# Kernel optimization log

Hardware: AMD Instinct MI355X
Metric: run time of the kernel (lower is better)

## Reference

```python
import jax, jax.numpy as jnp
import numpy as np

N = 100000      # nodes
E = 1600000     # edges (avg degree 16)
F_IN = 128
HID = 64
OUT = 40
NB = 10000      # batch_nodes
BN_EPS = 1e-5


def setup_inputs() -> dict:
    key = jax.random.key(0)
    ks = jax.random.split(key, 16)
    inp = {}
    inp["features"] = jax.random.normal(ks[0], (N, F_IN), dtype=jnp.float32)
    inp["edge_index"] = jax.random.randint(ks[1], (2, E), 0, N, dtype=jnp.int32)
    inp["batch_nodes"] = jax.random.randint(ks[2], (NB,), 0, N, dtype=jnp.int32)
    # conv1 params (Glorot-ish scale)
    inp["W1"] = jax.random.normal(ks[3], (F_IN, HID), dtype=jnp.float32) * (1.0 / np.sqrt(F_IN))
    inp["b1"] = jnp.zeros((HID,), jnp.float32)
    inp["k2_1"] = jnp.float32(0.5)   # learnable k^2, init 0.5
    # conv2 params
    inp["W2"] = jax.random.normal(ks[4], (HID, OUT), dtype=jnp.float32) * (1.0 / np.sqrt(HID))
    inp["b2"] = jnp.zeros((OUT,), jnp.float32)
    inp["k2_2"] = jnp.float32(0.5)
    # BatchNorm1d(hid) inference params
    inp["g1"] = jax.random.uniform(ks[5], (HID,), jnp.float32, 0.5, 1.5)
    inp["be1"] = jax.random.normal(ks[6], (HID,), jnp.float32) * 0.1
    inp["m1"] = jax.random.normal(ks[7], (HID,), jnp.float32) * 0.1
    inp["v1"] = jax.random.uniform(ks[8], (HID,), jnp.float32, 0.5, 1.5)
    # BatchNorm1d(out) inference params
    inp["g2"] = jax.random.uniform(ks[9], (OUT,), jnp.float32, 0.5, 1.5)
    inp["be2"] = jax.random.normal(ks[10], (OUT,), jnp.float32) * 0.1
    inp["m2"] = jax.random.normal(ks[11], (OUT,), jnp.float32) * 0.1
    inp["v2"] = jax.random.uniform(ks[12], (OUT,), jnp.float32, 0.5, 1.5)
    return inp


def _gcn_propagate(h, src, dst, n):
    # add self loops
    loop = jnp.arange(n, dtype=src.dtype)
    s = jnp.concatenate([src, loop])
    d = jnp.concatenate([dst, loop])
    # symmetric GCN normalization D^-1/2 A_hat D^-1/2
    deg = jnp.zeros((n,), h.dtype).at[d].add(1.0)
    dinv = jax.lax.rsqrt(deg)  # deg >= 1 thanks to self loops
    coef = dinv[s] * dinv[d]   # [E+N]
    msg = coef[:, None] * h[s]                      # gather  [E+N, C]
    agg = jnp.zeros_like(h).at[d].add(msg)          # scatter [N, C]
    return agg


def _helm_conv(x, W, b, k2, src, dst, n):
    h = x @ W                                   # [N, C_out]
    agg = _gcn_propagate(h, src, dst, n)        # A_hat h
    out = agg + k2 * h + b                      # (A_hat + k^2 I) h + b
    # Helmholtz residual: (A_hat - I + k^2 I) h ~ (-L + k^2) h
    resid = agg - h + k2 * h
    helm_loss = jnp.mean(resid * resid)
    return out, helm_loss


def _bn(x, g, be, m, v):
    return (x - m) * jax.lax.rsqrt(v + BN_EPS) * g + be


def reference(features, edge_index, batch_nodes, W1, b1, k2_1, W2, b2, k2_2,
              g1, be1, m1, v1, g2, be2, m2, v2):
    n = features.shape[0]
    src, dst = edge_index[0], edge_index[1]
    x, helm_loss1 = _helm_conv(features, W1, b1, k2_1, src, dst, n)
    x = jnp.tanh(_bn(x, g1, be1, m1, v1))
    # dropout is identity in eval mode
    x, _ = _helm_conv(x, W2, b2, k2_2, src, dst, n)
    x = jnp.tanh(_bn(x, g2, be2, m2, v2))
    logp = jax.nn.log_softmax(x[batch_nodes], axis=1)
    return (logp, helm_loss1)
```

## Files before the change

kernel.cpp:

```cpp
#include <hip/hip_runtime.h>
#include <math.h>


#define BN_EPS 1e-5f
#define NB_BKT 512
#define RCAP 4608
#define PSTRIDE 8448

typedef __attribute__((ext_vector_type(8))) short bf16x8;
typedef __attribute__((ext_vector_type(4))) float f32x4;

__device__ inline unsigned short f2b(float f) {
    unsigned u = __float_as_uint(f);
    unsigned r = (u + 0x7fffu + ((u >> 16) & 1u)) >> 16;
    return (unsigned short)r;
}
__device__ inline float b2f_lo(unsigned u) { return __uint_as_float(u << 16); }
__device__ inline float b2f_hi(unsigned u) { return __uint_as_float(u & 0xffff0000u); }
__device__ inline unsigned pk2(float a, float b) {
    return (unsigned)f2b(a) | ((unsigned)f2b(b) << 16);
}
__device__ inline float tanh_fast(float x) {
    float e = __expf(2.0f * x);
    return 1.0f - 2.0f * __builtin_amdgcn_rcpf(e + 1.0f);
}
__device__ inline float qcoef(unsigned q) {
    return __uint_as_float((q >> 1) & 0xFFFF0000u);
}

__global__ __launch_bounds__(256) void k_part(const int* __restrict__ src,
                                              const int* __restrict__ dst, int e,
                                              unsigned* __restrict__ bcnt,
                                              unsigned* __restrict__ part, int nblk) {
    __shared__ unsigned h[NB_BKT];
    __shared__ unsigned gbase[NB_BKT];
    __shared__ unsigned cur[NB_BKT];
    int chunk = ((e + nblk - 1) / nblk + 3) & ~3;
    int c0 = blockIdx.x * chunk;
    int c1 = min(c0 + chunk, e);
    if (c0 >= e) return;
    for (int i = threadIdx.x; i < NB_BKT; i += 256) h[i] = 0;
    __syncthreads();
    for (int i = c0 + threadIdx.x * 4; i < c1; i += 1024) {
        if (i + 3 < c1) {
            int4 d = *(const int4*)&dst[i];
            atomicAdd(&h[(unsigned)d.x >> 8], 1u);
            atomicAdd(&h[(unsigned)d.y >> 8], 1u);
            atomicAdd(&h[(unsigned)d.z >> 8], 1u);
            atomicAdd(&h[(unsigned)d.w >> 8], 1u);
        } else {
            for (int j = i; j < c1; ++j) atomicAdd(&h[(unsigned)dst[j] >> 8], 1u);
        }
    }
    __syncthreads();
    for (int i = threadIdx.x; i < NB_BKT; i += 256) {
        unsigned c = h[i];
        gbase[i] = c ? (i * RCAP + atomicAdd(&bcnt[i], c)) : 0u;
        cur[i] = 0;
    }
    __syncthreads();
    for (int i = c0 + threadIdx.x * 4; i < c1; i += 1024) {
        if (i + 3 < c1) {
            int4 s = *(const int4*)&src[i];
            int4 d = *(const int4*)&dst[i];
            unsigned b0 = (unsigned)d.x >> 8, b1 = (unsigned)d.y >> 8;
            unsigned b2 = (unsigned)d.z >> 8, b3 = (unsigned)d.w >> 8;
            unsigned p0 = gbase[b0] + atomicAdd(&cur[b0], 1u);
            unsigned p1 = gbase[b1] + atomicAdd(&cur[b1], 1u);
            unsigned p2 = gbase[b2] + atomicAdd(&cur[b2], 1u);
            unsigned p3 = gbase[b3] + atomicAdd(&cur[b3], 1u);
            if (p0 < (b0 + 1) * RCAP) part[p0] = (((unsigned)d.x & 255u) << 24) | (unsigned)s.x;
            if (p1 < (b1 + 1) * RCAP) part[p1] = (((unsigned)d.y & 255u) << 24) | (unsigned)s.y;
            if (p2 < (b2 + 1) * RCAP) part[p2] = (((unsigned)d.z & 255u) << 24) | (unsigned)s.z;
            if (p3 < (b3 + 1) * RCAP) part[p3] = (((unsigned)d.w & 255u) << 24) | (unsigned)s.w;
        } else {
            for (int j = i; j < c1; ++j) {
                unsigned b = (unsigned)dst[j] >> 8;
                unsigned p = gbase[b] + atomicAdd(&cur[b], 1u);
                if (p < (b + 1) * RCAP)
                    part[p] = (((unsigned)dst[j] & 255u) << 24) | (unsigned)src[j];
            }
        }
    }
}

__global__ __launch_bounds__(256) void k_deg(const unsigned* __restrict__ part,
                                             const unsigned* __restrict__ bcnt,
                                             unsigned long long* __restrict__ rowinfo,
                                             float* __restrict__ dinv, int n,
                                             const float* __restrict__ b1,
                                             const float* __restrict__ g1,
                                             const float* __restrict__ be1,
                                             const float* __restrict__ m1,
                                             const float* __restrict__ v1,
                                             const float* __restrict__ b2p,
                                             const float* __restrict__ g2,
                                             const float* __restrict__ be2,
                                             const float* __restrict__ m2,
                                             const float* __restrict__ v2,
                                             float* __restrict__ A1,
                                             float* __restrict__ S1,
                                             float* __restrict__ A2,
                                             float* __restrict__ S2) {
    __shared__ unsigned hist[256];
    __shared__ unsigned sc[256];
    int b = blockIdx.x;
    int cnt = (int)min(bcnt[b], (unsigned)RCAP);
    unsigned base = b * RCAP;
    int dst0 = b << 8;
    int nloc = min(256, n - dst0);
    int t = threadIdx.x;
    hist[t] = 0;
    __syncthreads();
    for (int i = t; i < cnt; i += 256) atomicAdd(&hist[part[base + i] >> 24], 1u);
    __syncthreads();
    unsigned c = hist[t];
    unsigned pcnt = (t < nloc) ? ((c + 15u) & ~15u) : 0u;
    sc[t] = pcnt;
    __syncthreads();
    for (int off = 1; off < 256; off <<= 1) {
        unsigned a = (t >= off) ? sc[t - off] : 0u;
        __syncthreads();
        sc[t] += a;
        __syncthreads();
    }
    if (t < nloc) {
        unsigned beg = (unsigned)b * PSTRIDE + (sc[t] - pcnt);
        rowinfo[dst0 + t] = (unsigned long long)beg | ((unsigned long long)pcnt << 32);
        dinv[dst0 + t] = rsqrtf((float)(c + 1u));
    }
    if (b == 0) {
        if (t < 64) {
            float a = g1[t] * rsqrtf(v1[t] + BN_EPS);
            A1[t] = a;
            S1[t] = (b1[t] - m1[t]) * a + be1[t];
        } else if (t < 104) {
            int cc = t - 64;
            float a = g2[cc] * rsqrtf(v2[cc] + BN_EPS);
            A2[cc] = a;
            S2[cc] = (b2p[cc] - m2[cc]) * a + be2[cc];
        }
    }
}

__global__ __launch_bounds__(256) void k_scatter(const unsigned* __restrict__ part,
                                                 const unsigned* __restrict__ bcnt,
                                                 const unsigned long long* __restrict__ rowinfo,
                                                 const float* __restrict__ dinv,
                                                 unsigned* __restrict__ qs, int n) {
    __shared__ unsigned cur[256];
    __shared__ unsigned pend[256];
    int b = blockIdx.x;
    int cnt = (int)min(bcnt[b], (unsigned)RCAP);
    unsigned base = b * RCAP;
    int dst0 = b << 8;
    int nloc = min(256, n - dst0);
    int t = threadIdx.x;
    if (t < nloc) {
        unsigned long long ri = rowinfo[dst0 + t];
        cur[t] = (unsigned)ri;
        pend[t] = (unsigned)ri + (unsigned)(ri >> 32);
    } else {
        cur[t] = 0;
        pend[t] = 0;
    }
    __syncthreads();
    for (int i = t; i < cnt; i += 256) {
        unsigned p = part[base + i];
        unsigned loc = p >> 24;
        unsigned s = p & 0xFFFFFFu;
        unsigned du = __float_as_uint(dinv[s]);
        unsigned q = (((du + 0x8000u) & 0xFFFF0000u) << 1) | s;
        unsigned pos = atomicAdd(&cur[loc], 1u);
        qs[pos] = q;
    }
    __syncthreads();
    if (t < nloc) {
        for (unsigned pos = cur[t]; pos < pend[t]; ++pos) qs[pos] = 0u;
    }
}

__global__ __launch_bounds__(256) void k_gemm1(const float* __restrict__ X,
                                               const float* __restrict__ W,
                                               unsigned* __restrict__ H, int n) {
    __shared__ short wb[4][4][64][8];
    __shared__ float cbuf[4][16][65];
    int t = threadIdx.x;
    for (int s = t; s < 1024; s += 256) {
        int l = s & 63, nt = (s >> 6) & 3, kt = s >> 8;
        int kbase = kt * 32 + ((l >> 4) << 3);
        int nn = nt * 16 + (l & 15);
        bf16x8 v;
#pragma unroll
        for (int j = 0; j < 8; ++j) v[j] = (short)f2b(W[(kbase + j) * 64 + nn]);
        *(bf16x8*)&wb[kt][nt][l][0] = v;
    }
    __syncthreads();
    int lane = t & 63, wave = t >> 6;
    int quad = lane >> 4, m = lane & 15;
    int r0 = blockIdx.x * 64 + wave * 16;
    f32x4 acc[4];
#pragma unroll
    for (int i = 0; i < 4; ++i) acc[i] = (f32x4){0.f, 0.f, 0.f, 0.f};
    int rr = min(r0 + m, n - 1);
    const float* xrow = X + (size_t)rr * 128;
#pragma unroll
    for (int kt = 0; kt < 4; ++kt) {
        int kb = kt * 32 + quad * 8;
        float4 x0 = *(const float4*)&xrow[kb];
        float4 x1 = *(const float4*)&xrow[kb + 4];
        bf16x8 af;
        af[0] = (short)f2b(x0.x); af[1] = (short)f2b(x0.y);
        af[2] = (short)f2b(x0.z); af[3] = (short)f2b(x0.w);
        af[4] = (short)f2b(x1.x); af[5] = (short)f2b(x1.y);
        af[6] = (short)f2b(x1.z); af[7] = (short)f2b(x1.w);
#pragma unroll
        for (int nt = 0; nt < 4; ++nt) {
            bf16x8 bf = *(bf16x8*)&wb[kt][nt][lane][0];
            acc[nt] = __builtin_amdgcn_mfma_f32_16x16x32_bf16(af, bf, acc[nt], 0, 0, 0);
        }
    }
#pragma unroll
    for (int nt = 0; nt < 4; ++nt)
#pragma unroll
        for (int r = 0; r < 4; ++r)
            cbuf[wave][quad * 4 + r][nt * 16 + m] = acc[nt][r];
    __syncthreads();
#pragma unroll
    for (int i = 0; i < 8; ++i) {
        int f = i * 64 + lane;
        int row = f >> 5, cp = f & 31;
        int grow = r0 + row;
        if (grow < n)
            H[(size_t)grow * 32 + cp] =
                pk2(cbuf[wave][row][2 * cp], cbuf[wave][row][2 * cp + 1]);
    }
}

__global__ __launch_bounds__(256) void k_gemm2(const unsigned short* __restrict__ X,
                                               const float* __restrict__ W,
                                               unsigned* __restrict__ H, int n) {
    __shared__ short wb[2][3][64][8];
    __shared__ float cbuf[4][16][49];
    int t = threadIdx.x;
    for (int s = t; s < 384; s += 256) {
        int l = s & 63, nt = (s >> 6) % 3, kt = s / 192;
        int kbase = kt * 32 + ((l >> 4) << 3);
        int c = nt * 16 + (l & 15);
        bf16x8 v;
#pragma unroll
        for (int j = 0; j < 8; ++j)
            v[j] = (c < 40) ? (short)f2b(W[(kbase + j) * 40 + c]) : (short)0;
        *(bf16x8*)&wb[kt][nt][l][0] = v;
    }
    __syncthreads();
    int lane = t & 63, wave = t >> 6;
    int quad = lane >> 4, m = lane & 15;
    int r0 = blockIdx.x * 64 + wave * 16;
    f32x4 acc[3];
#pragma unroll
    for (int i = 0; i < 3; ++i) acc[i] = (f32x4){0.f, 0.f, 0.f, 0.f};
    int rr = min(r0 + m, n - 1);
    const unsigned short* xrow = X + (size_t)rr * 64;
#pragma unroll
    for (int kt = 0; kt < 2; ++kt) {
        bf16x8 af = *(const bf16x8*)&xrow[kt * 32 + quad * 8];
#pragma unroll
        for (int nt = 0; nt < 3; ++nt) {
            bf16x8 bf = *(bf16x8*)&wb[kt][nt][lane][0];
            acc[nt] = __builtin_amdgcn_mfma_f32_16x16x32_bf16(af, bf, acc[nt], 0, 0, 0);
        }
    }
#pragma unroll
    for (int nt = 0; nt < 3; ++nt)
#pragma unroll
        for (int r = 0; r < 4; ++r)
            cbuf[wave][quad * 4 + r][nt * 16 + m] = acc[nt][r];
    __syncthreads();
#pragma unroll
    for (int i = 0; i < 5; ++i) {
        int f = i * 64 + lane;
        int row = f / 20, cp = f % 20;
        int grow = r0 + row;
        if (grow < n)
            H[(size_t)grow * 20 + cp] =
                pk2(cbuf[wave][row][2 * cp], cbuf[wave][row][2 * cp + 1]);
    }
}

__global__ __launch_bounds__(256) void k_conv1(const unsigned long long* __restrict__ rowinfo,
                                               const unsigned* __restrict__ qs,
                                               const float* __restrict__ dinv,
                                               const unsigned* __restrict__ h1,
                                               unsigned* __restrict__ x,
                                               const float* __restrict__ A1,
                                               const float* __restrict__ S1,
                                               const float* __restrict__ k2p,
                                               float* __restrict__ partial, int n) {
    int lane = threadIdx.x & 63, wave = threadIdx.x >> 6;
    int half = lane >> 5, c2 = lane & 31;
    int node = __builtin_amdgcn_readfirstlane(blockIdx.x * 4 + wave);
    float r2 = 0.0f;
    if (node < n) {
        unsigned long long ri = rowinfo[node];
        unsigned beg = (unsigned)ri, pdeg = (unsigned)(ri >> 32);
        float dd = dinv[node];
        unsigned hp = h1[(unsigned)node * 32u + (unsigned)c2];
        float hx = b2f_lo(hp), hy = b2f_hi(hp);
        float ax = half ? 0.f : dd * hx;
        float ay = half ? 0.f : dd * hy;
        for (unsigned eb = 0; eb < pdeg; eb += 16) {
            unsigned bi = beg + eb + (unsigned)half * 8u;
            uint4 q0 = *(const uint4*)&qs[bi];
            uint4 q1 = *(const uint4*)&qs[bi + 4];
            unsigned p0 = h1[((q0.x & 0x1FFFFu) << 5) + (unsigned)c2];
            unsigned p1 = h1[((q0.y & 0x1FFFFu) << 5) + (unsigned)c2];
            unsigned p2 = h1[((q0.z & 0x1FFFFu) << 5) + (unsigned)c2];
            unsigned p3 = h1[((q0.w & 0x1FFFFu) << 5) + (unsigned)c2];
            unsigned p4 = h1[((q1.x & 0x1FFFFu) << 5) + (unsigned)c2];
            unsigned p5 = h1[((q1.y & 0x1FFFFu) << 5) + (unsigned)c2];
            unsigned p6 = h1[((q1.z & 0x1FFFFu) << 5) + (unsigned)c2];
            unsigned p7 = h1[((q1.w & 0x1FFFFu) << 5) + (unsigned)c2];
            float c0 = qcoef(q0.x), c1 = qcoef(q0.y), c2f = qcoef(q0.z), c3 = qcoef(q0.w);
            float c4 = qcoef(q1.x), c5 = qcoef(q1.y), c6 = qcoef(q1.z), c7 = qcoef(q1.w);
            ax += c0 * b2f_lo(p0); ay += c0 * b2f_hi(p0);
            ax += c1 * b2f_lo(p1); ay += c1 * b2f_hi(p1);
            ax += c2f * b2f_lo(p2); ay += c2f * b2f_hi(p2);
            ax += c3 * b2f_lo(p3); ay += c3 * b2f_hi(p3);
            ax += c4 * b2f_lo(p4); ay += c4 * b2f_hi(p4);
            ax += c5 * b2f_lo(p5); ay += c5 * b2f_hi(p5);
            ax += c6 * b2f_lo(p6); ay += c6 * b2f_hi(p6);
            ax += c7 * b2f_lo(p7); ay += c7 * b2f_hi(p7);
        }
        ax += __shfl_xor(ax, 32, 64);
        ay += __shfl_xor(ay, 32, 64);
        if (half == 0) {
            float a_x = dd * ax, a_y = dd * ay;
            float k2 = k2p[0];
            float rx = a_x + (k2 - 1.0f) * hx;
            float ry = a_y + (k2 - 1.0f) * hy;
            r2 = rx * rx + ry * ry;
            float2 Ap = *(const float2*)&A1[2 * c2];
            float2 Sp = *(const float2*)&S1[2 * c2];
            float xnx = tanh_fast((a_x + k2 * hx) * Ap.x + Sp.x);
            float xny = tanh_fast((a_y + k2 * hy) * Ap.y + Sp.y);
            x[(unsigned)node * 32u + (unsigned)c2] = pk2(xnx, xny);
        }
    }
    for (int off = 32; off; off >>= 1) r2 += __shfl_xor(r2, off, 64);
    __shared__ float red[4];
    if (lane == 0) red[wave] = r2;
    __syncthreads();
    if (threadIdx.x == 0) partial[blockIdx.x] = red[0] + red[1] + red[2] + red[3];
}

__global__ __launch_bounds__(256) void k_conv2(const int* __restrict__ bn,
                                               const unsigned long long* __restrict__ rowinfo,
                                               const unsigned* __restrict__ qs,
                                               const float* __restrict__ dinv,
                                               const unsigned* __restrict__ h2,
                                               const float* __restrict__ A2,
                                               const float* __restrict__ S2,
                                               const float* __restrict__ k2p,
                                               const float* __restrict__ partial,
                                               int nparts, float inv_cnt,
                                               float* __restrict__ out, int nb) {
    int lane = threadIdx.x & 63, wave = threadIdx.x >> 6;
    if (blockIdx.x == gridDim.x - 1) {
        float s = 0.f;
        for (int i = threadIdx.x; i < nparts; i += 256) s += partial[i];
        for (int off = 32; off; off >>= 1) s += __shfl_xor(s, off, 64);
        __shared__ float red[4];
        if (lane == 0) red[wave] = s;
        __syncthreads();
        if (threadIdx.x == 0)
            out[(size_t)nb * 40] = (red[0] + red[1] + red[2] + red[3]) * inv_cnt;
        return;
    }
    int wid = blockIdx.x * 4 + wave;
    if (wid >= nb) return;
    int half = lane >> 5, c2 = lane & 31;
    unsigned p = (unsigned)min(c2, 19);
    int node = bn[wid];
    unsigned long long ri = rowinfo[node];
    unsigned beg = (unsigned)ri, pdeg = (unsigned)(ri >> 32);
    float dd = dinv[node];
    unsigned hp = h2[(unsigned)node * 20u + p];
    float hx = b2f_lo(hp), hy = b2f_hi(hp);
    float ax = half ? 0.f : dd * hx;
    float ay = half ? 0.f : dd * hy;
    for (unsigned eb = 0; eb < pdeg; eb += 16) {
        unsigned bi = beg + eb + (unsigned)half * 8u;
        uint4 q0 = *(const uint4*)&qs[bi];
        uint4 q1 = *(const uint4*)&qs[bi + 4];
        unsigned p0 = h2[(q0.x & 0x1FFFFu) * 20u + p];
        unsigned p1 = h2[(q0.y & 0x1FFFFu) * 20u + p];
        unsigned p2 = h2[(q0.z & 0x1FFFFu) * 20u + p];
        unsigned p3 = h2[(q0.w & 0x1FFFFu) * 20u + p];
        unsigned p4 = h2[(q1.x & 0x1FFFFu) * 20u + p];
        unsigned p5 = h2[(q1.y & 0x1FFFFu) * 20u + p];
        unsigned p6 = h2[(q1.z & 0x1FFFFu) * 20u + p];
        unsigned p7 = h2[(q1.w & 0x1FFFFu) * 20u + p];
        float c0 = qcoef(q0.x), c1 = qcoef(q0.y), c2f = qcoef(q0.z), c3 = qcoef(q0.w);
        float c4 = qcoef(q1.x), c5 = qcoef(q1.y), c6 = qcoef(q1.z), c7 = qcoef(q1.w);
        ax += c0 * b2f_lo(p0); ay += c0 * b2f_hi(p0);
        ax += c1 * b2f_lo(p1); ay += c1 * b2f_hi(p1);
        ax += c2f * b2f_lo(p2); ay += c2f * b2f_hi(p2);
        ax += c3 * b2f_lo(p3); ay += c3 * b2f_hi(p3);
        ax += c4 * b2f_lo(p4); ay += c4 * b2f_hi(p4);
        ax += c5 * b2f_lo(p5); ay += c5 * b2f_hi(p5);
        ax += c6 * b2f_lo(p6); ay += c6 * b2f_hi(p6);
        ax += c7 * b2f_lo(p7); ay += c7 * b2f_hi(p7);
    }
    ax += __shfl_xor(ax, 32, 64);
    ay += __shfl_xor(ay, 32, 64);
    float k2 = k2p[0];
    float2 Ap = *(const float2*)&A2[2 * p];
    float2 Sp = *(const float2*)&S2[2 * p];
    float tx = tanh_fast((dd * ax + k2 * hx) * Ap.x + Sp.x);
    float ty = tanh_fast((dd * ay + k2 * hy) * Ap.y + Sp.y);
    bool act = (half == 0) && (c2 < 20);
    float mx = act ? fmaxf(tx, ty) : -INFINITY;
    for (int off = 32; off; off >>= 1) mx = fmaxf(mx, __shfl_xor(mx, off, 64));
    float es = act ? (__expf(tx - mx) + __expf(ty - mx)) : 0.f;
    for (int off = 32; off; off >>= 1) es += __shfl_xor(es, off, 64);
    if (act) {
        float ls = mx + __logf(es);
        float2 o = make_float2(tx - ls, ty - ls);
        *(float2*)&out[(size_t)wid * 40 + 2 * p] = o;
    }
}

extern "C" void kernel_launch(void* const* d_in, const int* in_sizes, int n_in,
                              void* d_out, int out_size, void* d_ws, size_t ws_size,
                              hipStream_t stream) {
    const float* features = (const float*)d_in[0];
    const int* edge_index = (const int*)d_in[1];
    const int* batch_nodes = (const int*)d_in[2];
    const float* W1 = (const float*)d_in[3];
    const float* b1 = (const float*)d_in[4];
    const float* k2_1 = (const float*)d_in[5];
    const float* W2 = (const float*)d_in[6];
    const float* b2 = (const float*)d_in[7];
    const float* k2_2 = (const float*)d_in[8];
    const float* g1 = (const float*)d_in[9];
    const float* be1 = (const float*)d_in[10];
    const float* m1 = (const float*)d_in[11];
    const float* v1 = (const float*)d_in[12];
    const float* g2 = (const float*)d_in[13];
    const float* be2 = (const float*)d_in[14];
    const float* m2 = (const float*)d_in[15];
    const float* v2 = (const float*)d_in[16];

    const int N = in_sizes[0] / 128;
    const int E = in_sizes[1] / 2;
    const int NB = in_sizes[2];
    const int* src = edge_index;
    const int* dst = edge_index + E;
    const int NPART = (N + 3) / 4;
    const int NBKT = (N + 255) >> 8;
    const int PBLK = 512;

    unsigned* ws = (unsigned*)d_ws;
    auto align64 = [](size_t o) { return (o + 63) & ~(size_t)63; };
    size_t o = 0;
    unsigned long long* rowinfo = (unsigned long long*)(ws + o); o = align64(o + 2 * (size_t)N);
    float* dinv = (float*)(ws + o);       o = align64(o + N);
    float* A1 = (float*)(ws + o);         o = align64(o + 64);
    float* S1 = (float*)(ws + o);         o = align64(o + 64);
    float* A2 = (float*)(ws + o);         o = align64(o + 64);
    float* S2 = (float*)(ws + o);         o = align64(o + 64);
    unsigned* bcnt = ws + o;              o = align64(o + NB_BKT);
    float* partial = (float*)(ws + o);    o = align64(o + NPART);
    unsigned* qs = ws + o;                o = align64(o + (size_t)NB_BKT * PSTRIDE);
    unsigned* h1 = ws + o;                o = align64(o + (size_t)N * 32);
    unsigned* x = ws + o;                 o = align64(o + (size_t)N * 32);
    unsigned* h2 = ws + o;                o = align64(o + (size_t)N * 20);
    unsigned* part = h1;

    hipMemsetAsync(bcnt, 0, NB_BKT * sizeof(unsigned), stream);
    k_part<<<PBLK, 256, 0, stream>>>(src, dst, E, bcnt, part, PBLK);
    k_deg<<<NBKT, 256, 0, stream>>>(part, bcnt, rowinfo, dinv, N, b1, g1, be1, m1,
                                    v1, b2, g2, be2, m2, v2, A1, S1, A2, S2);
    k_scatter<<<NBKT, 256, 0, stream>>>(part, bcnt, rowinfo, dinv, qs, N);

    k_gemm1<<<(N + 63) / 64, 256, 0, stream>>>(features, W1, h1, N);
    k_conv1<<<NPART, 256, 0, stream>>>(rowinfo, qs, dinv, h1, x, A1, S1, k2_1,
                                       partial, N);
    k_gemm2<<<(N + 63) / 64, 256, 0, stream>>>((const unsigned short*)x, W2, h2, N);
    k_conv2<<<(NB + 3) / 4 + 1, 256, 0, stream>>>(batch_nodes, rowinfo, qs, dinv, h2,
                                                  A2, S2, k2_2, partial, NPART,
                                                  1.0f / ((float)N * 64.0f),
                                                  (float*)d_out, NB);
}
```

Measured before the change: 259.6 us.

## Fuse edge scatter with gemm1 and shrink per-node padding in aggregation

Merges the edge scatter kernel and the first GEMM into one launch whose leading blocks do the scatter and whose remaining blocks do the GEMM. This requires giving the partition buffer its own workspace region instead of aliasing h1. Per-node edge padding drops from multiples of 16 to multiples of 4, and both conv kernels are restructured: conv1 assigns a 16-lane group per node, and conv2 assigns a half-wave per batch node. The goal is to cut wasted padded-edge work and a kernel boundary. The cost is narrower per-node loops with less memory-level parallelism per thread, and fewer partition blocks.

```diff
diff --git a/kernel.cpp b/kernel.cpp
--- a/kernel.cpp
+++ b/kernel.cpp
@@ -5,7 +5,7 @@
 #define BN_EPS 1e-5f
 #define NB_BKT 512
 #define RCAP 4608
-#define PSTRIDE 8448
+#define PSTRIDE 5376
 
 typedef __attribute__((ext_vector_type(8))) short bf16x8;
 typedef __attribute__((ext_vector_type(4))) float f32x4;
@@ -115,7 +115,7 @@
     for (int i = t; i < cnt; i += 256) atomicAdd(&hist[part[base + i] >> 24], 1u);
     __syncthreads();
     unsigned c = hist[t];
-    unsigned pcnt = (t < nloc) ? ((c + 15u) & ~15u) : 0u;
+    unsigned pcnt = (t < nloc) ? ((c + 3u) & ~3u) : 0u;
     sc[t] = pcnt;
     __syncthreads();
     for (int off = 1; off < 256; off <<= 1) {
@@ -143,49 +143,48 @@
     }
 }
 
-__global__ __launch_bounds__(256) void k_scatter(const unsigned* __restrict__ part,
-                                                 const unsigned* __restrict__ bcnt,
-                                                 const unsigned long long* __restrict__ rowinfo,
-                                                 const float* __restrict__ dinv,
-                                                 unsigned* __restrict__ qs, int n) {
-    __shared__ unsigned cur[256];
-    __shared__ unsigned pend[256];
-    int b = blockIdx.x;
-    int cnt = (int)min(bcnt[b], (unsigned)RCAP);
-    unsigned base = b * RCAP;
-    int dst0 = b << 8;
-    int nloc = min(256, n - dst0);
+__global__ __launch_bounds__(256) void k_scatter_gemm1(
+        const unsigned* __restrict__ part, const unsigned* __restrict__ bcnt,
+        const unsigned long long* __restrict__ rowinfo,
+        const float* __restrict__ dinv, unsigned* __restrict__ qs,
+        const float* __restrict__ X, const float* __restrict__ W,
+        unsigned* __restrict__ H, int n, int nbkt) {
+    __shared__ union {
+        struct { unsigned cur[256]; unsigned pend[256]; } s;
+        struct { short wb[4][4][64][8]; float cbuf[4][16][65]; } g;
+    } u;
     int t = threadIdx.x;
-    if (t < nloc) {
-        unsigned long long ri = rowinfo[dst0 + t];
-        cur[t] = (unsigned)ri;
-        pend[t] = (unsigned)ri + (unsigned)(ri >> 32);
-    } else {
-        cur[t] = 0;
-        pend[t] = 0;
-    }
-    __syncthreads();
-    for (int i = t; i < cnt; i += 256) {
-        unsigned p = part[base + i];
-        unsigned loc = p >> 24;
-        unsigned s = p & 0xFFFFFFu;
-        unsigned du = __float_as_uint(dinv[s]);
-        unsigned q = (((du + 0x8000u) & 0xFFFF0000u) << 1) | s;
-        unsigned pos = atomicAdd(&cur[loc], 1u);
-        qs[pos] = q;
-    }
-    __syncthreads();
-    if (t < nloc) {
-        for (unsigned pos = cur[t]; pos < pend[t]; ++pos) qs[pos] = 0u;
-    }
-}
-
-__global__ __launch_bounds__(256) void k_gemm1(const float* __restrict__ X,
-                                               const float* __restrict__ W,
-                                               unsigned* __restrict__ H, int n) {
-    __shared__ short wb[4][4][64][8];
-    __shared__ float cbuf[4][16][65];
-    int t = threadIdx.x;
+    if (blockIdx.x < (unsigned)nbkt) {
+        int b = blockIdx.x;
+        int cnt = (int)min(bcnt[b], (unsigned)RCAP);
+        unsigned base = b * RCAP;
+        int dst0 = b << 8;
+        int nloc = min(256, n - dst0);
+        if (t < nloc) {
+            unsigned long long ri = rowinfo[dst0 + t];
+            u.s.cur[t] = (unsigned)ri;
+            u.s.pend[t] = (unsigned)ri + (unsigned)(ri >> 32);
+        } else {
+            u.s.cur[t] = 0;
+            u.s.pend[t] = 0;
+        }
+        __syncthreads();
+        for (int i = t; i < cnt; i += 256) {
+            unsigned p = part[base + i];
+            unsigned loc = p >> 24;
+            unsigned s = p & 0xFFFFFFu;
+            unsigned du = __float_as_uint(dinv[s]);
+            unsigned q = (((du + 0x8000u) & 0xFFFF0000u) << 1) | s;
+            unsigned pos = atomicAdd(&u.s.cur[loc], 1u);
+            qs[pos] = q;
+        }
+        __syncthreads();
+        if (t < nloc) {
+            for (unsigned pos = u.s.cur[t]; pos < u.s.pend[t]; ++pos) qs[pos] = 0u;
+        }
+        return;
+    }
+    int bid = blockIdx.x - nbkt;
     for (int s = t; s < 1024; s += 256) {
         int l = s & 63, nt = (s >> 6) & 3, kt = s >> 8;
         int kbase = kt * 32 + ((l >> 4) << 3);
@@ -193,12 +192,12 @@
         bf16x8 v;
 #pragma unroll
         for (int j = 0; j < 8; ++j) v[j] = (short)f2b(W[(kbase + j) * 64 + nn]);
-        *(bf16x8*)&wb[kt][nt][l][0] = v;
+        *(bf16x8*)&u.g.wb[kt][nt][l][0] = v;
     }
     __syncthreads();
     int lane = t & 63, wave = t >> 6;
     int quad = lane >> 4, m = lane & 15;
-    int r0 = blockIdx.x * 64 + wave * 16;
+    int r0 = bid * 64 + wave * 16;
     f32x4 acc[4];
 #pragma unroll
     for (int i = 0; i < 4; ++i) acc[i] = (f32x4){0.f, 0.f, 0.f, 0.f};
@@ -216,7 +215,7 @@
         af[6] = (short)f2b(x1.z); af[7] = (short)f2b(x1.w);
 #pragma unroll
         for (int nt = 0; nt < 4; ++nt) {
-            bf16x8 bf = *(bf16x8*)&wb[kt][nt][lane][0];
+            bf16x8 bf = *(bf16x8*)&u.g.wb[kt][nt][lane][0];
             acc[nt] = __builtin_amdgcn_mfma_f32_16x16x32_bf16(af, bf, acc[nt], 0, 0, 0);
         }
     }
@@ -224,7 +223,7 @@
     for (int nt = 0; nt < 4; ++nt)
 #pragma unroll
         for (int r = 0; r < 4; ++r)
-            cbuf[wave][quad * 4 + r][nt * 16 + m] = acc[nt][r];
+            u.g.cbuf[wave][quad * 4 + r][nt * 16 + m] = acc[nt][r];
     __syncthreads();
 #pragma unroll
     for (int i = 0; i < 8; ++i) {
@@ -233,7 +232,7 @@
         int grow = r0 + row;
         if (grow < n)
             H[(size_t)grow * 32 + cp] =
-                pk2(cbuf[wave][row][2 * cp], cbuf[wave][row][2 * cp + 1]);
+                pk2(u.g.cbuf[wave][row][2 * cp], u.g.cbuf[wave][row][2 * cp + 1]);
     }
 }
 
@@ -297,61 +296,58 @@
                                                const float* __restrict__ S1,
                                                const float* __restrict__ k2p,
                                                float* __restrict__ partial, int n) {
-    int lane = threadIdx.x & 63, wave = threadIdx.x >> 6;
-    int half = lane >> 5, c2 = lane & 31;
-    int node = __builtin_amdgcn_readfirstlane(blockIdx.x * 4 + wave);
+    int t = threadIdx.x;
+    int lane = t & 63, wave = t >> 6;
+    int quarter = lane >> 4, cl = lane & 15;
+    int node = blockIdx.x * 16 + wave * 4 + quarter;
     float r2 = 0.0f;
     if (node < n) {
         unsigned long long ri = rowinfo[node];
         unsigned beg = (unsigned)ri, pdeg = (unsigned)(ri >> 32);
         float dd = dinv[node];
-        unsigned hp = h1[(unsigned)node * 32u + (unsigned)c2];
-        float hx = b2f_lo(hp), hy = b2f_hi(hp);
-        float ax = half ? 0.f : dd * hx;
-        float ay = half ? 0.f : dd * hy;
-        for (unsigned eb = 0; eb < pdeg; eb += 16) {
-            unsigned bi = beg + eb + (unsigned)half * 8u;
-            uint4 q0 = *(const uint4*)&qs[bi];
-            uint4 q1 = *(const uint4*)&qs[bi + 4];
-            unsigned p0 = h1[((q0.x & 0x1FFFFu) << 5) + (unsigned)c2];
-            unsigned p1 = h1[((q0.y & 0x1FFFFu) << 5) + (unsigned)c2];
-            unsigned p2 = h1[((q0.z & 0x1FFFFu) << 5) + (unsigned)c2];
-            unsigned p3 = h1[((q0.w & 0x1FFFFu) << 5) + (unsigned)c2];
-            unsigned p4 = h1[((q1.x & 0x1FFFFu) << 5) + (unsigned)c2];
-            unsigned p5 = h1[((q1.y & 0x1FFFFu) << 5) + (unsigned)c2];
-            unsigned p6 = h1[((q1.z & 0x1FFFFu) << 5) + (unsigned)c2];
-            unsigned p7 = h1[((q1.w & 0x1FFFFu) << 5) + (unsigned)c2];
-            float c0 = qcoef(q0.x), c1 = qcoef(q0.y), c2f = qcoef(q0.z), c3 = qcoef(q0.w);
-            float c4 = qcoef(q1.x), c5 = qcoef(q1.y), c6 = qcoef(q1.z), c7 = qcoef(q1.w);
-            ax += c0 * b2f_lo(p0); ay += c0 * b2f_hi(p0);
-            ax += c1 * b2f_lo(p1); ay += c1 * b2f_hi(p1);
-            ax += c2f * b2f_lo(p2); ay += c2f * b2f_hi(p2);
-            ax += c3 * b2f_lo(p3); ay += c3 * b2f_hi(p3);
-            ax += c4 * b2f_lo(p4); ay += c4 * b2f_hi(p4);
-            ax += c5 * b2f_lo(p5); ay += c5 * b2f_hi(p5);
-            ax += c6 * b2f_lo(p6); ay += c6 * b2f_hi(p6);
-            ax += c7 * b2f_lo(p7); ay += c7 * b2f_hi(p7);
-        }
-        ax += __shfl_xor(ax, 32, 64);
-        ay += __shfl_xor(ay, 32, 64);
-        if (half == 0) {
-            float a_x = dd * ax, a_y = dd * ay;
-            float k2 = k2p[0];
-            float rx = a_x + (k2 - 1.0f) * hx;
-            float ry = a_y + (k2 - 1.0f) * hy;
-            r2 = rx * rx + ry * ry;
-            float2 Ap = *(const float2*)&A1[2 * c2];
-            float2 Sp = *(const float2*)&S1[2 * c2];
-            float xnx = tanh_fast((a_x + k2 * hx) * Ap.x + Sp.x);
-            float xny = tanh_fast((a_y + k2 * hy) * Ap.y + Sp.y);
-            x[(unsigned)node * 32u + (unsigned)c2] = pk2(xnx, xny);
-        }
+        uint2 hp = *(const uint2*)&h1[(unsigned)node * 32u + 2u * cl];
+        float h0 = b2f_lo(hp.x), h1v = b2f_hi(hp.x);
+        float h2v = b2f_lo(hp.y), h3 = b2f_hi(hp.y);
+        float a0 = dd * h0, a1 = dd * h1v, a2 = dd * h2v, a3 = dd * h3;
+        for (unsigned eb = 0; eb < pdeg; eb += 4) {
+            uint4 q = *(const uint4*)&qs[beg + eb];
+            unsigned i0 = (q.x & 0x1FFFFu) << 5, i1 = (q.y & 0x1FFFFu) << 5;
+            unsigned i2 = (q.z & 0x1FFFFu) << 5, i3 = (q.w & 0x1FFFFu) << 5;
+            uint2 p0 = *(const uint2*)&h1[i0 + 2u * cl];
+            uint2 p1 = *(const uint2*)&h1[i1 + 2u * cl];
+            uint2 p2 = *(const uint2*)&h1[i2 + 2u * cl];
+            uint2 p3 = *(const uint2*)&h1[i3 + 2u * cl];
+            float c0 = qcoef(q.x), c1 = qcoef(q.y), c2 = qcoef(q.z), c3 = qcoef(q.w);
+            a0 += c0 * b2f_lo(p0.x); a1 += c0 * b2f_hi(p0.x);
+            a2 += c0 * b2f_lo(p0.y); a3 += c0 * b2f_hi(p0.y);
+            a0 += c1 * b2f_lo(p1.x); a1 += c1 * b2f_hi(p1.x);
+            a2 += c1 * b2f_lo(p1.y); a3 += c1 * b2f_hi(p1.y);
+            a0 += c2 * b2f_lo(p2.x); a1 += c2 * b2f_hi(p2.x);
+            a2 += c2 * b2f_lo(p2.y); a3 += c2 * b2f_hi(p2.y);
+            a0 += c3 * b2f_lo(p3.x); a1 += c3 * b2f_hi(p3.x);
+            a2 += c3 * b2f_lo(p3.y); a3 += c3 * b2f_hi(p3.y);
+        }
+        float k2 = k2p[0];
+        float g0 = dd * a0, g1v = dd * a1, g2v = dd * a2, g3 = dd * a3;
+        float r0 = g0 + (k2 - 1.0f) * h0, r1 = g1v + (k2 - 1.0f) * h1v;
+        float r2c = g2v + (k2 - 1.0f) * h2v, r3 = g3 + (k2 - 1.0f) * h3;
+        r2 = r0 * r0 + r1 * r1 + r2c * r2c + r3 * r3;
+        float4 Ap = *(const float4*)&A1[4 * cl];
+        float4 Sp = *(const float4*)&S1[4 * cl];
+        float x0 = tanh_fast((g0 + k2 * h0) * Ap.x + Sp.x);
+        float x1 = tanh_fast((g1v + k2 * h1v) * Ap.y + Sp.y);
+        float x2 = tanh_fast((g2v + k2 * h2v) * Ap.z + Sp.z);
+        float x3 = tanh_fast((g3 + k2 * h3) * Ap.w + Sp.w);
+        uint2 o;
+        o.x = pk2(x0, x1);
+        o.y = pk2(x2, x3);
+        *(uint2*)&x[(unsigned)node * 32u + 2u * cl] = o;
     }
     for (int off = 32; off; off >>= 1) r2 += __shfl_xor(r2, off, 64);
     __shared__ float red[4];
     if (lane == 0) red[wave] = r2;
     __syncthreads();
-    if (threadIdx.x == 0) partial[blockIdx.x] = red[0] + red[1] + red[2] + red[3];
+    if (t == 0) partial[blockIdx.x] = red[0] + red[1] + red[2] + red[3];
 }
 
 __global__ __launch_bounds__(256) void k_conv2(const int* __restrict__ bn,
@@ -377,53 +373,39 @@
             out[(size_t)nb * 40] = (red[0] + red[1] + red[2] + red[3]) * inv_cnt;
         return;
     }
-    int wid = blockIdx.x * 4 + wave;
+    int half = lane >> 5, p32 = lane & 31;
+    unsigned p = (unsigned)min(p32, 19);
+    int wid = blockIdx.x * 8 + wave * 2 + half;
     if (wid >= nb) return;
-    int half = lane >> 5, c2 = lane & 31;
-    unsigned p = (unsigned)min(c2, 19);
     int node = bn[wid];
     unsigned long long ri = rowinfo[node];
     unsigned beg = (unsigned)ri, pdeg = (unsigned)(ri >> 32);
     float dd = dinv[node];
     unsigned hp = h2[(unsigned)node * 20u + p];
     float hx = b2f_lo(hp), hy = b2f_hi(hp);
-    float ax = half ? 0.f : dd * hx;
-    float ay = half ? 0.f : dd * hy;
-    for (unsigned eb = 0; eb < pdeg; eb += 16) {
-        unsigned bi = beg + eb + (unsigned)half * 8u;
-        uint4 q0 = *(const uint4*)&qs[bi];
-        uint4 q1 = *(const uint4*)&qs[bi + 4];
-        unsigned p0 = h2[(q0.x & 0x1FFFFu) * 20u + p];
-        unsigned p1 = h2[(q0.y & 0x1FFFFu) * 20u + p];
-        unsigned p2 = h2[(q0.z & 0x1FFFFu) * 20u + p];
-        unsigned p3 = h2[(q0.w & 0x1FFFFu) * 20u + p];
-        unsigned p4 = h2[(q1.x & 0x1FFFFu) * 20u + p];
-        unsigned p5 = h2[(q1.y & 0x1FFFFu) * 20u + p];
-        unsigned p6 = h2[(q1.z & 0x1FFFFu) * 20u + p];
-        unsigned p7 = h2[(q1.w & 0x1FFFFu) * 20u + p];
-        float c0 = qcoef(q0.x), c1 = qcoef(q0.y), c2f = qcoef(q0.z), c3 = qcoef(q0.w);
-        float c4 = qcoef(q1.x), c5 = qcoef(q1.y), c6 = qcoef(q1.z), c7 = qcoef(q1.w);
-        ax += c0 * b2f_lo(p0); ay += c0 * b2f_hi(p0);
-        ax += c1 * b2f_lo(p1); ay += c1 * b2f_hi(p1);
-        ax += c2f * b2f_lo(p2); ay += c2f * b2f_hi(p2);
-        ax += c3 * b2f_lo(p3); ay += c3 * b2f_hi(p3);
-        ax += c4 * b2f_lo(p4); ay += c4 * b2f_hi(p4);
-        ax += c5 * b2f_lo(p5); ay += c5 * b2f_hi(p5);
-        ax += c6 * b2f_lo(p6); ay += c6 * b2f_hi(p6);
-        ax += c7 * b2f_lo(p7); ay += c7 * b2f_hi(p7);
-    }
-    ax += __shfl_xor(ax, 32, 64);
-    ay += __shfl_xor(ay, 32, 64);
+    float ax = dd * hx, ay = dd * hy;
+    for (unsigned eb = 0; eb < pdeg; eb += 4) {
+        uint4 q = *(const uint4*)&qs[beg + eb];
+        unsigned pv0 = h2[(q.x & 0x1FFFFu) * 20u + p];
+        unsigned pv1 = h2[(q.y & 0x1FFFFu) * 20u + p];
+        unsigned pv2 = h2[(q.z & 0x1FFFFu) * 20u + p];
+        unsigned pv3 = h2[(q.w & 0x1FFFFu) * 20u + p];
+        float c0 = qcoef(q.x), c1 = qcoef(q.y), c2 = qcoef(q.z), c3 = qcoef(q.w);
+        ax += c0 * b2f_lo(pv0); ay += c0 * b2f_hi(pv0);
+        ax += c1 * b2f_lo(pv1); ay += c1 * b2f_hi(pv1);
+        ax += c2 * b2f_lo(pv2); ay += c2 * b2f_hi(pv2);
+        ax += c3 * b2f_lo(pv3); ay += c3 * b2f_hi(pv3);
+    }
     float k2 = k2p[0];
     float2 Ap = *(const float2*)&A2[2 * p];
     float2 Sp = *(const float2*)&S2[2 * p];
     float tx = tanh_fast((dd * ax + k2 * hx) * Ap.x + Sp.x);
     float ty = tanh_fast((dd * ay + k2 * hy) * Ap.y + Sp.y);
-    bool act = (half == 0) && (c2 < 20);
+    bool act = (p32 < 20);
     float mx = act ? fmaxf(tx, ty) : -INFINITY;
-    for (int off = 32; off; off >>= 1) mx = fmaxf(mx, __shfl_xor(mx, off, 64));
+    for (int off = 16; off; off >>= 1) mx = fmaxf(mx, __shfl_xor(mx, off, 32));
     float es = act ? (__expf(tx - mx) + __expf(ty - mx)) : 0.f;
-    for (int off = 32; off; off >>= 1) es += __shfl_xor(es, off, 64);
+    for (int off = 16; off; off >>= 1) es += __shfl_xor(es, off, 32);
     if (act) {
         float ls = mx + __logf(es);
         float2 o = make_float2(tx - ls, ty - ls);
@@ -457,9 +439,10 @@
     const int NB = in_sizes[2];
     const int* src = edge_index;
     const int* dst = edge_index + E;
-    const int NPART = (N + 3) / 4;
+    const int NPART = (N + 15) / 16;
     const int NBKT = (N + 255) >> 8;
-    const int PBLK = 512;
+    const int PBLK = 256;
+    const int GEMM1B = (N + 63) / 64;
 
     unsigned* ws = (unsigned*)d_ws;
     auto align64 = [](size_t o) { return (o + 63) & ~(size_t)63; };
@@ -476,19 +459,18 @@
     unsigned* h1 = ws + o;                o = align64(o + (size_t)N * 32);
     unsigned* x = ws + o;                 o = align64(o + (size_t)N * 32);
     unsigned* h2 = ws + o;                o = align64(o + (size_t)N * 20);
-    unsigned* part = h1;
+    unsigned* part = ws + o;              o = align64(o + (size_t)NB_BKT * RCAP);
 
     hipMemsetAsync(bcnt, 0, NB_BKT * sizeof(unsigned), stream);
     k_part<<<PBLK, 256, 0, stream>>>(src, dst, E, bcnt, part, PBLK);
     k_deg<<<NBKT, 256, 0, stream>>>(part, bcnt, rowinfo, dinv, N, b1, g1, be1, m1,
                                     v1, b2, g2, be2, m2, v2, A1, S1, A2, S2);
-    k_scatter<<<NBKT, 256, 0, stream>>>(part, bcnt, rowinfo, dinv, qs, N);
-
-    k_gemm1<<<(N + 63) / 64, 256, 0, stream>>>(features, W1, h1, N);
+    k_scatter_gemm1<<<NBKT + GEMM1B, 256, 0, stream>>>(part, bcnt, rowinfo, dinv,
+                                                       qs, features, W1, h1, N, NBKT);
     k_conv1<<<NPART, 256, 0, stream>>>(rowinfo, qs, dinv, h1, x, A1, S1, k2_1,
                                        partial, N);
     k_gemm2<<<(N + 63) / 64, 256, 0, stream>>>((const unsigned short*)x, W2, h2, N);
-    k_conv2<<<(NB + 3) / 4 + 1, 256, 0, stream>>>(batch_nodes, rowinfo, qs, dinv, h2,
+    k_conv2<<<(NB + 7) / 8 + 1, 256, 0, stream>>>(batch_nodes, rowinfo, qs, dinv, h2,
                                                   A2, S2, k2_2, partial, NPART,
                                                   1.0f / ((float)N * 64.0f),
                                                   (float*)d_out, NB);
```

Measured after the change: 221.3 us. -14.7%, faster.
